# Optimization experiments

Hardware: AMD Instinct MI355X
Metric: run time of the kernel (lower is better)

Reference implementation:

```python
import jax, jax.numpy as jnp
import numpy as np

N_QUBITS = 4
N_LAYERS = 3
INV_SQRT2 = 0.7071067811865476
BSZ = 262144


def _apply_ry(state, wire, theta):
    # state: [B,2,2,2,2] complex; theta: [B] (per-batch rotation angle)
    s = jnp.moveaxis(state, wire + 1, -1)
    a0, a1 = s[..., 0], s[..., 1]
    c = jnp.cos(theta * 0.5)[:, None, None, None]
    sn = jnp.sin(theta * 0.5)[:, None, None, None]
    out = jnp.stack([c * a0 - sn * a1, sn * a0 + c * a1], axis=-1)
    return jnp.moveaxis(out, -1, wire + 1)


def _apply_h(state, wire):
    s = jnp.moveaxis(state, wire + 1, -1)
    a0, a1 = s[..., 0], s[..., 1]
    out = jnp.stack([(a0 + a1) * INV_SQRT2, (a0 - a1) * INV_SQRT2], axis=-1)
    return jnp.moveaxis(out, -1, wire + 1)


def _apply_crz(state, cw, tw, phi):
    # controlled-RZ: phase exp(-/+ i*phi/2) on |c=1,t=0/1>; phi is a scalar param
    s = jnp.moveaxis(state, (cw + 1, tw + 1), (-2, -1))
    phase = jnp.exp(1j * phi * jnp.array([-0.5, 0.5], dtype=jnp.float32)).astype(s.dtype)
    s = s.at[..., 1, :].multiply(phase)
    return jnp.moveaxis(s, (-2, -1), (cw + 1, tw + 1))


def _circuit(angles, weights):
    # angles: [B,4]; weights: [12]; returns PauliZ expvals [B,4]
    B = angles.shape[0]
    state = jnp.zeros((B, 2, 2, 2, 2), jnp.complex64).at[:, 0, 0, 0, 0].set(1.0)
    for i in range(N_QUBITS):
        state = _apply_ry(state, i, angles[:, i])
    for l in range(N_LAYERS):
        lp = weights[N_QUBITS * l: N_QUBITS * (l + 1)]
        for i in range(N_QUBITS):
            state = _apply_crz(state, i, (i + 1) % N_QUBITS, lp[i])
        for i in range(N_QUBITS):
            state = _apply_h(state, i)
    p = state.real ** 2 + state.imag ** 2  # [B,2,2,2,2] probabilities
    z = jnp.stack(
        [jnp.take(p, 0, axis=w + 1).sum(axis=(1, 2, 3))
         - jnp.take(p, 1, axis=w + 1).sum(axis=(1, 2, 3))
         for w in range(N_QUBITS)],
        axis=-1,
    )
    return z


def setup_inputs() -> dict:
    key = jax.random.key(0)
    k1, k2, k3, k4 = jax.random.split(key, 4)
    x = jax.random.uniform(k1, (BSZ, 16), dtype=jnp.float32)
    weights = jax.random.normal(k2, (N_LAYERS * N_QUBITS,), dtype=jnp.float32)
    lin_w = jax.random.normal(k3, (2, 16), dtype=jnp.float32) * 0.25
    lin_b = jax.random.normal(k4, (2,), dtype=jnp.float32) * 0.1
    return {"x": x, "weights": weights, "lin_w": lin_w, "lin_b": lin_b}


def reference(x, weights, lin_w, lin_b):
    bsz = x.shape[0]
    # 4x4 image -> four 2x2 patches in loop order (0,0),(0,2),(2,0),(2,2);
    # each patch flattened row-major: [x[j,k], x[j,k+1], x[j+1,k], x[j+1,k+1]]
    xv = x.reshape(bsz, 2, 2, 2, 2).transpose(0, 1, 3, 2, 4).reshape(bsz * 4, 4)
    q = _circuit(xv, weights).reshape(bsz, 16)  # patch-major feature order as in torch cat
    logits = q @ lin_w.T + lin_b
    return jax.nn.softmax(logits, axis=1)
```

## Files before the change

### kernel.cpp

```cpp
#include <hip/hip_runtime.h>


__device__ __forceinline__ float layer_angle(const float* __restrict__ w,
                                             int l, int idx) {
    float ang = 0.f;
    #pragma unroll
    for (int g = 0; g < 4; ++g) {
        int cb = (idx >> (3 - g)) & 1;
        int tb = (idx >> (3 - ((g + 1) & 3))) & 1;
        if (cb) ang += (tb ? 0.5f : -0.5f) * w[l * 4 + g];
    }
    return ang;
}

__global__ __launch_bounds__(256) void precompute_tensors(
    const float* __restrict__ weights,
    const float* __restrict__ lin_w,
    float* __restrict__ ws)
{
    __shared__ float2 U1[256], U2[256], U[256];
    __shared__ float zeta[4][16];
    __shared__ float G[4][256];
    __shared__ float A[4][3][64];
    __shared__ float B[4][9][16];
    __shared__ float C1[4][27][4];
    int t = threadIdx.x;
    int i = t >> 4, j = t & 15;

    {
        float sgn = (__popc(i & j) & 1) ? -1.f : 1.f;
        float a = layer_angle(weights, 0, j);
        U1[t] = make_float2(sgn * __cosf(a), sgn * __sinf(a));
    }
    if (t < 64) {
        int s = t >> 4, k = t & 15;
        float z = 0.f;
        #pragma unroll
        for (int w = 0; w < 4; ++w) {
            float sg = ((k >> (3 - w)) & 1) ? -1.f : 1.f;
            z += (lin_w[s * 4 + w] - lin_w[16 + s * 4 + w]) * sg;
        }
        zeta[s][k] = z;
    }
    __syncthreads();
    {
        float ar = 0.f, ai = 0.f;
        for (int k = 0; k < 16; ++k) {
            float sgn = (__popc(i & k) & 1) ? -1.f : 1.f;
            float a = layer_angle(weights, 1, k);
            float cr = sgn * __cosf(a), ci = sgn * __sinf(a);
            float2 u = U1[k * 16 + j];
            ar += cr * u.x - ci * u.y;
            ai += cr * u.y + ci * u.x;
        }
        U2[t] = make_float2(ar, ai);
    }
    __syncthreads();
    {
        float ar = 0.f, ai = 0.f;
        for (int k = 0; k < 16; ++k) {
            float sgn = (__popc(i & k) & 1) ? -1.f : 1.f;
            float a = layer_angle(weights, 2, k);
            float cr = sgn * __cosf(a), ci = sgn * __sinf(a);
            float2 u = U2[k * 16 + j];
            ar += cr * u.x - ci * u.y;
            ai += cr * u.y + ci * u.x;
        }
        U[t] = make_float2(ar, ai);
    }
    __syncthreads();
    {
        float g[4] = {0, 0, 0, 0};
        for (int k = 0; k < 16; ++k) {
            float2 uki = U[k * 16 + i], ukj = U[k * 16 + j];
            float p = uki.x * ukj.x + uki.y * ukj.y;
            #pragma unroll
            for (int s = 0; s < 4; ++s) g[s] += zeta[s][k] * p;
        }
        #pragma unroll
        for (int s = 0; s < 4; ++s) G[s][t] = g[s];
    }
    __syncthreads();
    for (int e = t; e < 768; e += 256) {
        int m = e / 192, r = e % 192;
        int t3 = r / 64, q = r % 64;
        int ih = q >> 3, jh = q & 7;
        float g00 = G[m][(ih * 2 + 0) * 16 + jh * 2 + 0];
        float g01 = G[m][(ih * 2 + 0) * 16 + jh * 2 + 1];
        float g10 = G[m][(ih * 2 + 1) * 16 + jh * 2 + 0];
        float g11 = G[m][(ih * 2 + 1) * 16 + jh * 2 + 1];
        A[m][t3][q] = (t3 == 0) ? g00 + g11 : (t3 == 1) ? g00 - g11 : g01 + g10;
    }
    __syncthreads();
    for (int e = t; e < 576; e += 256) {
        int m = e / 144, r = e % 144;
        int t2 = r / 48; r %= 48;
        int t3 = r / 16, q = r % 16;
        int ih = q >> 2, jh = q & 3;
        float a00 = A[m][t3][(ih * 2 + 0) * 8 + jh * 2 + 0];
        float a01 = A[m][t3][(ih * 2 + 0) * 8 + jh * 2 + 1];
        float a10 = A[m][t3][(ih * 2 + 1) * 8 + jh * 2 + 0];
        float a11 = A[m][t3][(ih * 2 + 1) * 8 + jh * 2 + 1];
        B[m][t2 * 3 + t3][q] = (t2 == 0) ? a00 + a11
                             : (t2 == 1) ? a00 - a11 : a01 + a10;
    }
    __syncthreads();
    for (int e = t; e < 432; e += 256) {
        int m = e / 108, r = e % 108;
        int t1 = r / 36; r %= 36;
        int t23 = r / 4, q = r % 4;
        int ih = q >> 1, jh = q & 1;
        float b00 = B[m][t23][(ih * 2 + 0) * 4 + jh * 2 + 0];
        float b01 = B[m][t23][(ih * 2 + 0) * 4 + jh * 2 + 1];
        float b10 = B[m][t23][(ih * 2 + 1) * 4 + jh * 2 + 0];
        float b11 = B[m][t23][(ih * 2 + 1) * 4 + jh * 2 + 1];
        C1[m][t1 * 9 + t23][q] = (t1 == 0) ? b00 + b11
                               : (t1 == 1) ? b00 - b11 : b01 + b10;
    }
    __syncthreads();
    const float scale = 1.f / 65536.f;
    for (int e = t; e < 324; e += 256) {
        int m = e / 81, r = e % 81;
        int t0 = r / 27, t123 = r % 27;
        const float* c = C1[m][t123];
        float v = (t0 == 0) ? c[0] + c[3] : (t0 == 1) ? c[0] - c[3]
                                          : c[1] + c[2];
        ws[m * 81 + r] = v * scale;
    }
}

__global__ __launch_bounds__(256) void qcircuit_kernel(
    const float* __restrict__ x,
    const float* __restrict__ lin_b,
    const float* __restrict__ tab,
    float* __restrict__ out,
    int nrows)
{
    int b = blockIdx.x * blockDim.x + threadIdx.x;
    if (b >= nrows) return;

    const float* xr = x + (size_t)b * 16;
    float4 xa = *(const float4*)(xr);
    float4 xb = *(const float4*)(xr + 4);
    float4 xc = *(const float4*)(xr + 8);
    float4 xd = *(const float4*)(xr + 12);
    float xs[16] = {xa.x, xa.y, xa.z, xa.w, xb.x, xb.y, xb.z, xb.w,
                    xc.x, xc.y, xc.z, xc.w, xd.x, xd.y, xd.z, xd.w};
    float cs[16], sn[16];
    #pragma unroll
    for (int i = 0; i < 16; ++i) __sincosf(xs[i], &sn[i], &cs[i]);

    float d = 0.f;
    #pragma unroll
    for (int s = 0; s < 4; ++s) {
        int b0 = ((s >> 1) << 3) + ((s & 1) << 1);
        float W[3] = {1.f, cs[b0],     sn[b0]};
        float X[3] = {1.f, cs[b0 + 1], sn[b0 + 1]};
        float C2 = cs[b0 + 4], S2 = sn[b0 + 4];
        float C3 = cs[b0 + 5], S3 = sn[b0 + 5];
        const float* T = tab + s * 81;
        #pragma unroll
        for (int t0 = 0; t0 < 3; ++t0) {
            float a0 = 0.f;
            #pragma unroll
            for (int t1 = 0; t1 < 3; ++t1) {
                const float* T3 = T + t0 * 27 + t1 * 9;
                float u0 = T3[0] + C3 * T3[1] + S3 * T3[2];
                float u1 = T3[3] + C3 * T3[4] + S3 * T3[5];
                float u2 = T3[6] + C3 * T3[7] + S3 * T3[8];
                float a1 = u0 + C2 * u1 + S2 * u2;
                a0 += X[t1] * a1;
            }
            d += W[t0] * a0;
        }
    }

    d += lin_b[0] - lin_b[1];
    float p0 = 1.f / (1.f + __expf(-d));
    *(float2*)(out + (size_t)b * 2) = make_float2(p0, 1.f - p0);
}

extern "C" void kernel_launch(void* const* d_in, const int* in_sizes, int n_in,
                              void* d_out, int out_size, void* d_ws, size_t ws_size,
                              hipStream_t stream) {
    const float* x       = (const float*)d_in[0];
    const float* weights = (const float*)d_in[1];
    const float* lin_w   = (const float*)d_in[2];
    const float* lin_b   = (const float*)d_in[3];
    float* out = (float*)d_out;
    float* ws  = (float*)d_ws;

    int nrows = in_sizes[0] / 16;

    precompute_tensors<<<1, 256, 0, stream>>>(weights, lin_w, ws);

    int block = 256;
    int grid = (nrows + block - 1) / block;
    qcircuit_kernel<<<grid, block, 0, stream>>>(x, lin_b, ws, out, nrows);
}
```

Baseline: 77.94 us.

## Fuse table precompute into main kernel, process four rows per thread with packed float2 math

Merges the single-block precompute kernel into the main kernel, so every block rebuilds the 324-entry contraction table in shared memory while its x loads are already in flight. Each thread now handles four rows and packs pairs of rows into float2 FMAs, and the bias is folded into the table. This removes a kernel launch and the serialized dependency on a one-block kernel. The cost is that all 256 blocks redundantly repeat the table construction, plus higher register pressure from holding four rows of inputs.

```diff
diff --git a/kernel.cpp b/kernel.cpp
--- a/kernel.cpp
+++ b/kernel.cpp
@@ -13,10 +13,96 @@
     return ang;
 }
 
-__global__ __launch_bounds__(256) void precompute_tensors(
+__device__ __forceinline__ float2 f2fmas(float2 a, float b, float2 c) {
+    return make_float2(fmaf(a.x, b, c.x), fmaf(a.y, b, c.y));
+}
+__device__ __forceinline__ float2 f2fma(float2 a, float2 b, float2 c) {
+    return make_float2(fmaf(a.x, b.x, c.x), fmaf(a.y, b.y, c.y));
+}
+__device__ __forceinline__ float2 f2add(float2 a, float2 b) {
+    return make_float2(a.x + b.x, a.y + b.y);
+}
+
+__device__ __forceinline__ void compute_chunk(
+    const float4 (&xv)[4][4],
+    const float (&tabs)[4][9][12],
+    float* __restrict__ out,
+    int base, int nrows, int t)
+{
+    float2 d[2] = {make_float2(0.f, 0.f), make_float2(0.f, 0.f)};
+
+    #pragma unroll
+    for (int s = 0; s < 4; ++s) {
+        float2 C0[2], S0[2], C1v[2], S1[2], C2[2], S2[2], C3[2], S3[2];
+        #pragma unroll
+        for (int r = 0; r < 4; ++r) {
+            const int lo = (s >> 1) * 2;
+            float4 va = xv[r][lo], vb = xv[r][lo + 1];
+            float a0, a1, a2, a3;
+            if (s & 1) { a0 = va.z; a1 = va.w; a2 = vb.z; a3 = vb.w; }
+            else       { a0 = va.x; a1 = va.y; a2 = vb.x; a3 = vb.y; }
+            const int p = r >> 1;
+            float c, sn;
+            __sincosf(a0, &sn, &c);
+            if (r & 1) { C0[p].y = c;  S0[p].y = sn; } else { C0[p].x = c;  S0[p].x = sn; }
+            __sincosf(a1, &sn, &c);
+            if (r & 1) { C1v[p].y = c; S1[p].y = sn; } else { C1v[p].x = c; S1[p].x = sn; }
+            __sincosf(a2, &sn, &c);
+            if (r & 1) { C2[p].y = c;  S2[p].y = sn; } else { C2[p].x = c;  S2[p].x = sn; }
+            __sincosf(a3, &sn, &c);
+            if (r & 1) { C3[p].y = c;  S3[p].y = sn; } else { C3[p].x = c;  S3[p].x = sn; }
+        }
+
+        #pragma unroll
+        for (int t0 = 0; t0 < 3; ++t0) {
+            float2 acc[2] = {make_float2(0.f, 0.f), make_float2(0.f, 0.f)};
+            #pragma unroll
+            for (int t1 = 0; t1 < 3; ++t1) {
+                const float* tp = &tabs[s][t0 * 3 + t1][0];
+                float4 q0 = *(const float4*)tp;
+                float4 q1 = *(const float4*)(tp + 4);
+                float  k8 = tp[8];
+                #pragma unroll
+                for (int p = 0; p < 2; ++p) {
+                    float2 u0 = f2fmas(S3[p], q0.z,
+                                 f2fmas(C3[p], q0.y, make_float2(q0.x, q0.x)));
+                    float2 u1 = f2fmas(S3[p], q1.y,
+                                 f2fmas(C3[p], q1.x, make_float2(q0.w, q0.w)));
+                    float2 u2 = f2fmas(S3[p], k8,
+                                 f2fmas(C3[p], q1.w, make_float2(q1.z, q1.z)));
+                    float2 a1v = f2fma(S2[p], u2, f2fma(C2[p], u1, u0));
+                    if      (t1 == 0) acc[p] = f2add(acc[p], a1v);
+                    else if (t1 == 1) acc[p] = f2fma(C1v[p], a1v, acc[p]);
+                    else              acc[p] = f2fma(S1[p],  a1v, acc[p]);
+                }
+            }
+            #pragma unroll
+            for (int p = 0; p < 2; ++p) {
+                if      (t0 == 0) d[p] = f2add(d[p], acc[p]);
+                else if (t0 == 1) d[p] = f2fma(C0[p], acc[p], d[p]);
+                else              d[p] = f2fma(S0[p], acc[p], d[p]);
+            }
+        }
+    }
+
+    #pragma unroll
+    for (int r = 0; r < 4; ++r) {
+        int row = base + r * 256 + t;
+        if (row < nrows) {
+            float dv = (r & 1) ? d[r >> 1].y : d[r >> 1].x;
+            float p0 = 1.f / (1.f + __expf(-dv));
+            *(float2*)(out + (size_t)row * 2) = make_float2(p0, 1.f - p0);
+        }
+    }
+}
+
+__global__ __launch_bounds__(256) void fused_qcircuit(
+    const float* __restrict__ x,
     const float* __restrict__ weights,
     const float* __restrict__ lin_w,
-    float* __restrict__ ws)
+    const float* __restrict__ lin_b,
+    float* __restrict__ out,
+    int nrows)
 {
     __shared__ float2 U1[256], U2[256], U[256];
     __shared__ float zeta[4][16];
@@ -24,8 +110,21 @@
     __shared__ float A[4][3][64];
     __shared__ float B[4][9][16];
     __shared__ float C1[4][27][4];
+    __shared__ __align__(16) float tabs[4][9][12];
+
     int t = threadIdx.x;
     int i = t >> 4, j = t & 15;
+
+    int base = blockIdx.x * 1024;
+    float4 xv[4][4];
+    #pragma unroll
+    for (int r = 0; r < 4; ++r) {
+        int row = base + r * 256 + t;
+        int rc = row < nrows ? row : 0;
+        const float4* xp = (const float4*)(x + (size_t)rc * 16);
+        xv[r][0] = xp[0]; xv[r][1] = xp[1]; xv[r][2] = xp[2]; xv[r][3] = xp[3];
+    }
+    float bias = lin_b[0] - lin_b[1];
 
     {
         float sgn = (__popc(i & j) & 1) ? -1.f : 1.f;
@@ -118,66 +217,34 @@
                                : (t1 == 1) ? b00 - b11 : b01 + b10;
     }
     __syncthreads();
-    const float scale = 1.f / 65536.f;
-    for (int e = t; e < 324; e += 256) {
-        int m = e / 81, r = e % 81;
-        int t0 = r / 27, t123 = r % 27;
-        const float* c = C1[m][t123];
-        float v = (t0 == 0) ? c[0] + c[3] : (t0 == 1) ? c[0] - c[3]
-                                          : c[1] + c[2];
-        ws[m * 81 + r] = v * scale;
-    }
-}
-
-__global__ __launch_bounds__(256) void qcircuit_kernel(
-    const float* __restrict__ x,
-    const float* __restrict__ lin_b,
-    const float* __restrict__ tab,
-    float* __restrict__ out,
-    int nrows)
-{
-    int b = blockIdx.x * blockDim.x + threadIdx.x;
-    if (b >= nrows) return;
-
-    const float* xr = x + (size_t)b * 16;
-    float4 xa = *(const float4*)(xr);
-    float4 xb = *(const float4*)(xr + 4);
-    float4 xc = *(const float4*)(xr + 8);
-    float4 xd = *(const float4*)(xr + 12);
-    float xs[16] = {xa.x, xa.y, xa.z, xa.w, xb.x, xb.y, xb.z, xb.w,
-                    xc.x, xc.y, xc.z, xc.w, xd.x, xd.y, xd.z, xd.w};
-    float cs[16], sn[16];
-    #pragma unroll
-    for (int i = 0; i < 16; ++i) __sincosf(xs[i], &sn[i], &cs[i]);
-
-    float d = 0.f;
-    #pragma unroll
-    for (int s = 0; s < 4; ++s) {
-        int b0 = ((s >> 1) << 3) + ((s & 1) << 1);
-        float W[3] = {1.f, cs[b0],     sn[b0]};
-        float X[3] = {1.f, cs[b0 + 1], sn[b0 + 1]};
-        float C2 = cs[b0 + 4], S2 = sn[b0 + 4];
-        float C3 = cs[b0 + 5], S3 = sn[b0 + 5];
-        const float* T = tab + s * 81;
-        #pragma unroll
-        for (int t0 = 0; t0 < 3; ++t0) {
-            float a0 = 0.f;
-            #pragma unroll
-            for (int t1 = 0; t1 < 3; ++t1) {
-                const float* T3 = T + t0 * 27 + t1 * 9;
-                float u0 = T3[0] + C3 * T3[1] + S3 * T3[2];
-                float u1 = T3[3] + C3 * T3[4] + S3 * T3[5];
-                float u2 = T3[6] + C3 * T3[7] + S3 * T3[8];
-                float a1 = u0 + C2 * u1 + S2 * u2;
-                a0 += X[t1] * a1;
-            }
-            d += W[t0] * a0;
-        }
-    }
-
-    d += lin_b[0] - lin_b[1];
-    float p0 = 1.f / (1.f + __expf(-d));
-    *(float2*)(out + (size_t)b * 2) = make_float2(p0, 1.f - p0);
+    {
+        const float scale = 1.f / 65536.f;
+        for (int e = t; e < 324; e += 256) {
+            int m = e / 81, r = e % 81;
+            int t0 = r / 27, t123 = r % 27;
+            const float* c = C1[m][t123];
+            float v = (t0 == 0) ? c[0] + c[3] : (t0 == 1) ? c[0] - c[3]
+                                              : c[1] + c[2];
+            float val = v * scale;
+            if (e == 0) val += bias;
+            int t1 = t123 / 9, k = t123 % 9;
+            tabs[m][t0 * 3 + t1][k] = val;
+        }
+    }
+    __syncthreads();
+
+    compute_chunk(xv, tabs, out, base, nrows, t);
+
+    for (base += gridDim.x * 1024; base < nrows; base += gridDim.x * 1024) {
+        #pragma unroll
+        for (int r = 0; r < 4; ++r) {
+            int row = base + r * 256 + t;
+            int rc = row < nrows ? row : 0;
+            const float4* xp = (const float4*)(x + (size_t)rc * 16);
+            xv[r][0] = xp[0]; xv[r][1] = xp[1]; xv[r][2] = xp[2]; xv[r][3] = xp[3];
+        }
+        compute_chunk(xv, tabs, out, base, nrows, t);
+    }
 }
 
 extern "C" void kernel_launch(void* const* d_in, const int* in_sizes, int n_in,
@@ -188,13 +255,9 @@
     const float* lin_w   = (const float*)d_in[2];
     const float* lin_b   = (const float*)d_in[3];
     float* out = (float*)d_out;
-    float* ws  = (float*)d_ws;
 
     int nrows = in_sizes[0] / 16;
-
-    precompute_tensors<<<1, 256, 0, stream>>>(weights, lin_w, ws);
-
-    int block = 256;
-    int grid = (nrows + block - 1) / block;
-    qcircuit_kernel<<<grid, block, 0, stream>>>(x, lin_b, ws, out, nrows);
-}
+    int grid = (nrows + 1023) / 1024;
+    if (grid < 1) grid = 1;
+    fused_qcircuit<<<grid, 256, 0, stream>>>(x, weights, lin_w, lin_b, out, nrows);
+}
```

New measurement: 76.09 us. -2.4%, faster.
